# Optimization experiments

Measured on AMD Instinct MI355X. Metric: run time of the kernel, lower is better.

## Reference

```python
import jax, jax.numpy as jnp
import numpy as np

N = 98304        # total nodes (= 16384 graphs * act_dim 6)
E = 1572864      # edges (avg degree 16)
C = 64           # in_channels
H = 32           # hidden_size
ACT = 6          # act_dim


def setup_inputs() -> dict:
    key = jax.random.key(0)
    ks = jax.random.split(key, 11)
    s = lambda fan: 1.0 / np.sqrt(fan)
    return {
        "state": jax.random.normal(ks[0], (N, C), jnp.float32),
        "edge_index": jax.random.randint(ks[1], (2, E), 0, N, dtype=jnp.int64),
        "conv_W": jax.random.normal(ks[2], (C, C), jnp.float32) * s(C),
        "conv_b": jax.random.normal(ks[3], (C,), jnp.float32) * 0.01,
        "W1": jax.random.normal(ks[4], (C, H), jnp.float32) * s(C),
        "b1": jax.random.normal(ks[5], (H,), jnp.float32) * 0.01,
        "W2": jax.random.normal(ks[6], (H, H), jnp.float32) * s(H),
        "b2": jax.random.normal(ks[7], (H,), jnp.float32) * 0.01,
        "W3": jax.random.normal(ks[8], (H, 1), jnp.float32) * s(H),
        "b3": jax.random.normal(ks[9], (1,), jnp.float32) * 0.01,
    }


def gcn_conv(x, edge_index, W, b):
    # PyG GCNConv: add self-loops, symmetric normalization D^-1/2 (A+I) D^-1/2 (X W) + b
    loops = jnp.arange(N, dtype=edge_index.dtype)
    src = jnp.concatenate([edge_index[0], loops])  # [E+N]
    dst = jnp.concatenate([edge_index[1], loops])  # [E+N]
    deg = jax.ops.segment_sum(jnp.ones(E + N, x.dtype), dst, num_segments=N)
    dinv = jax.lax.rsqrt(deg)                      # deg >= 1 due to self-loops
    norm = dinv[src] * dinv[dst]                   # [E+N]
    h = x @ W                                      # [N, C]
    msg = h[src] * norm[:, None]                   # gather + scale
    return jax.ops.segment_sum(msg, dst, num_segments=N) + b


def reference(state, edge_index, conv_W, conv_b, W1, b1, W2, b2, W3, b3):
    out = jax.nn.relu(gcn_conv(state, edge_index, conv_W, conv_b))
    x = out + state                                # residual
    x = x.reshape(-1, ACT, C)                      # [num_graphs, act_dim, C]
    x = jax.nn.relu(x @ W1 + b1)
    x = jax.nn.relu(x @ W2 + b2)
    x = jax.nn.softplus(x @ W3 + b3)
    concentration = x.squeeze(-1) + 1e-20          # [num_graphs, act_dim]
    return concentration
```

## Files before the change

kernel.cpp:

```cpp
#include <hip/hip_runtime.h>
#include <math.h>

#define Nn 98304
#define Ee 1572864
#define Cc 64
#define Hh 32
#define TT 128
#define NT (Nn / TT)
#define HB 128
#define EPB (Ee / HB)
#define CAPT 2560


__device__ __forceinline__ int detect64(const void* ei) {
    const unsigned int* u = (const unsigned int*)ei;
    int is64 = 1;
    #pragma unroll
    for (int i = 0; i < 16; ++i) is64 &= (u[2 * i + 1] == 0u);
    return is64;
}

__device__ __forceinline__ int load_idx(const void* ei, long e, int is64) {
    if (is64) return (int)((const long long*)ei)[e];
    return ((const int*)ei)[e];
}

__device__ __forceinline__ unsigned short f2bf(float x) {
    union { float f; unsigned int u; } v; v.f = x;
    unsigned int r = v.u + 0x7FFFu + ((v.u >> 16) & 1u);
    return (unsigned short)(r >> 16);
}
__device__ __forceinline__ float bf2f(unsigned short h) {
    union { unsigned int u; float f; } v; v.u = ((unsigned int)h) << 16;
    return v.f;
}

__global__ __launch_bounds__(1024) void k_bucket(const void* __restrict__ ei,
                                                 unsigned int* __restrict__ aux,
                                                 unsigned int* __restrict__ ebuf) {
    __shared__ unsigned int hl[NT];
    __shared__ unsigned int off[NT];
    int t = threadIdx.x, b = blockIdx.x;
    if (t < NT) hl[t] = 0;
    __syncthreads();
    int is64 = detect64(ei);
    long e0 = (long)b * EPB;
    #pragma unroll
    for (int i = 0; i < EPB / 1024; ++i) {
        int d = load_idx(ei, (long)Ee + e0 + i * 1024 + t, is64);
        atomicAdd(&hl[d >> 7], 1u);
    }
    __syncthreads();
    if (t < NT) off[t] = hl[t];
    __syncthreads();
    for (int s = 1; s < NT; s <<= 1) {
        unsigned int v = (t < NT && t >= s) ? off[t - s] : 0u;
        __syncthreads();
        if (t < NT) off[t] += v;
        __syncthreads();
    }
    if (t < NT) {
        unsigned int ex = off[t] - hl[t];
        aux[(long)b * NT + t] = ex | (hl[t] << 16);
        off[t] = ex;
    }
    __syncthreads();
    #pragma unroll
    for (int i = 0; i < EPB / 1024; ++i) {
        long e = e0 + i * 1024 + t;
        int s = load_idx(ei, e, is64);
        int d = load_idx(ei, (long)Ee + e, is64);
        unsigned int pos = atomicAdd(&off[d >> 7], 1u);
        ebuf[(long)b * EPB + pos] = (unsigned int)s | ((unsigned int)(d & (TT - 1)) << 17);
    }
}

__global__ __launch_bounds__(256) void k_nodecnt(const unsigned int* __restrict__ aux,
                                                 const unsigned int* __restrict__ ebuf,
                                                 unsigned int* __restrict__ rowOff,
                                                 unsigned int* __restrict__ rowEnd,
                                                 float* __restrict__ dinv,
                                                 unsigned int* __restrict__ srcs) {
    __shared__ unsigned int stage[CAPT];
    __shared__ unsigned int rbI[HB];
    __shared__ unsigned int ro[HB];
    __shared__ unsigned int cnt[TT];
    __shared__ unsigned int sc[TT];
    __shared__ unsigned int cur[TT];
    int t = threadIdx.x, tile = blockIdx.x;
    if (t < HB) {
        unsigned int av = aux[(long)t * NT + tile];
        ro[t] = av & 0xFFFFu;
        rbI[t] = av >> 16;
    }
    __syncthreads();
    for (int s = 1; s < HB; s <<= 1) {
        unsigned int v = (t < HB && t >= s) ? rbI[t - s] : 0u;
        __syncthreads();
        if (t < HB) rbI[t] += v;
        __syncthreads();
    }
    int total = (int)rbI[HB - 1];
    for (int i = t; i < total; i += 256) {
        int pos = 0;
        #pragma unroll
        for (int s = HB / 2; s > 0; s >>= 1)
            if ((int)rbI[pos + s - 1] <= i) pos += s;
        unsigned int prev = pos ? rbI[pos - 1] : 0u;
        stage[i] = ebuf[(long)pos * EPB + ro[pos] + (unsigned int)i - prev];
    }
    if (t < TT) cnt[t] = 0;
    __syncthreads();
    for (int i = t; i < total; i += 256)
        atomicAdd(&cnt[stage[i] >> 17], 1u);
    __syncthreads();
    if (t < TT) sc[t] = cnt[t];
    __syncthreads();
    #pragma unroll
    for (int off = 1; off < TT; off <<= 1) {
        unsigned int v = (t >= off && t < TT) ? sc[t - off] : 0u;
        __syncthreads();
        if (t < TT) sc[t] += v;
        __syncthreads();
    }
    if (t < TT) {
        unsigned int start = (unsigned int)(tile * CAPT) + sc[t] - cnt[t];
        rowOff[(long)tile * TT + t] = start;
        rowEnd[(long)tile * TT + t] = start + cnt[t];
        cur[t] = start;
        dinv[(long)tile * TT + t] = rsqrtf((float)(cnt[t] + 1));
    }
    __syncthreads();
    for (int i = t; i < total; i += 256) {
        unsigned int u = stage[i];
        unsigned int pos = atomicAdd(&cur[u >> 17], 1u);
        srcs[pos] = u & 0x1FFFFu;
    }
}

__global__ __launch_bounds__(256) void k_gemm(const float* __restrict__ state,
                                              const float* __restrict__ W,
                                              const float* __restrict__ dinv,
                                              unsigned short* __restrict__ gb) {
    __shared__ float Wl[64 * 64];
    __shared__ float Al[64 * 68];
    int t = threadIdx.x;
    long n0 = (long)blockIdx.x * 64;

    const float4* W4 = (const float4*)W;
    float4* Wl4 = (float4*)Wl;
    #pragma unroll
    for (int i = 0; i < 4; ++i) Wl4[i * 256 + t] = W4[i * 256 + t];

    const float4* S4 = (const float4*)(state) + n0 * 16;
    #pragma unroll
    for (int i = 0; i < 4; ++i) {
        int f4 = t + i * 256;
        int r = f4 >> 4, k0 = (f4 & 15) * 4;
        *(float4*)(Al + r * 68 + k0) = S4[f4];
    }
    __syncthreads();

    int r0 = (t >> 4) * 4;
    int c0 = (t & 15) * 4;
    float acc[4][4] = {{0.f}};
    #pragma unroll
    for (int kk = 0; kk < 64; kk += 4) {
        float4 a4[4], w4[4];
        #pragma unroll
        for (int i = 0; i < 4; ++i) a4[i] = *(const float4*)(Al + (r0 + i) * 68 + kk);
        #pragma unroll
        for (int j = 0; j < 4; ++j) w4[j] = *(const float4*)(Wl + (kk + j) * 64 + c0);
        const float* aa = (const float*)a4;
        const float* ww = (const float*)w4;
        #pragma unroll
        for (int i = 0; i < 4; ++i)
            #pragma unroll
            for (int j = 0; j < 4; ++j) {
                float av = aa[i * 4 + j];
                #pragma unroll
                for (int c = 0; c < 4; ++c)
                    acc[i][c] = fmaf(av, ww[j * 4 + c], acc[i][c]);
            }
    }
    #pragma unroll
    for (int i = 0; i < 4; ++i) {
        long n = n0 + r0 + i;
        float dv = dinv[n];
        ushort4 o;
        o.x = f2bf(acc[i][0] * dv); o.y = f2bf(acc[i][1] * dv);
        o.z = f2bf(acc[i][2] * dv); o.w = f2bf(acc[i][3] * dv);
        *(ushort4*)(gb + n * 64 + c0) = o;
    }
}

__global__ __launch_bounds__(256) void k_gather(const unsigned int* __restrict__ rowOff,
                                                const unsigned int* __restrict__ rowEnd,
                                                const unsigned int* __restrict__ srcs,
                                                const unsigned short* __restrict__ gb,
                                                const float* __restrict__ dinv,
                                                float* __restrict__ agg) {
    int wave = threadIdx.x >> 6, lane = threadIdx.x & 63;
    int n = blockIdx.x * 4 + wave;
    int start = (int)rowOff[n];
    int end = (int)rowEnd[n];
    float acc = bf2f(gb[(long)n * 64 + lane]);
    for (int base = start; base < end; base += 64) {
        int m = min(64, end - base);
        int sv = (lane < m) ? (int)srcs[base + lane] : 0;
        int j = 0;
        for (; j + 8 <= m; j += 8) {
            int s0 = __shfl(sv, j,     64);
            int s1 = __shfl(sv, j + 1, 64);
            int s2 = __shfl(sv, j + 2, 64);
            int s3 = __shfl(sv, j + 3, 64);
            int s4 = __shfl(sv, j + 4, 64);
            int s5 = __shfl(sv, j + 5, 64);
            int s6 = __shfl(sv, j + 6, 64);
            int s7 = __shfl(sv, j + 7, 64);
            float v0 = bf2f(gb[(long)s0 * 64 + lane]);
            float v1 = bf2f(gb[(long)s1 * 64 + lane]);
            float v2 = bf2f(gb[(long)s2 * 64 + lane]);
            float v3 = bf2f(gb[(long)s3 * 64 + lane]);
            float v4 = bf2f(gb[(long)s4 * 64 + lane]);
            float v5 = bf2f(gb[(long)s5 * 64 + lane]);
            float v6 = bf2f(gb[(long)s6 * 64 + lane]);
            float v7 = bf2f(gb[(long)s7 * 64 + lane]);
            acc += ((v0 + v1) + (v2 + v3)) + ((v4 + v5) + (v6 + v7));
        }
        for (; j + 4 <= m; j += 4) {
            int s0 = __shfl(sv, j,     64);
            int s1 = __shfl(sv, j + 1, 64);
            int s2 = __shfl(sv, j + 2, 64);
            int s3 = __shfl(sv, j + 3, 64);
            float v0 = bf2f(gb[(long)s0 * 64 + lane]);
            float v1 = bf2f(gb[(long)s1 * 64 + lane]);
            float v2 = bf2f(gb[(long)s2 * 64 + lane]);
            float v3 = bf2f(gb[(long)s3 * 64 + lane]);
            acc += (v0 + v1) + (v2 + v3);
        }
        for (; j < m; ++j) {
            int s = __shfl(sv, j, 64);
            acc += bf2f(gb[(long)s * 64 + lane]);
        }
    }
    agg[(long)n * 64 + lane] = acc * dinv[n];
}

__global__ __launch_bounds__(256) void k_final(const float* __restrict__ agg,
                                               const float* __restrict__ state,
                                               const float* __restrict__ conv_b,
                                               const float* __restrict__ W1,
                                               const float* __restrict__ b1,
                                               const float* __restrict__ W2,
                                               const float* __restrict__ b2,
                                               const float* __restrict__ W3,
                                               const float* __restrict__ b3,
                                               float* __restrict__ out) {
    __shared__ float sW1[Cc * Hh];
    __shared__ float sW2[Hh * Hh];
    __shared__ float sW3[Hh], sb1[Hh], sb2[Hh], scb[Cc];
    __shared__ float sb3;
    int t = threadIdx.x;
    for (int i = t; i < Cc * Hh; i += 256) sW1[i] = W1[i];
    for (int i = t; i < Hh * Hh; i += 256) sW2[i] = W2[i];
    if (t < Hh) { sW3[t] = W3[t]; sb1[t] = b1[t]; sb2[t] = b2[t]; }
    if (t < Cc) scb[t] = conv_b[t];
    if (t == 0) sb3 = b3[0];
    __syncthreads();

    int n = blockIdx.x * 256 + t;
    const float4* a4p = (const float4*)(agg + (long)n * 64);
    const float4* s4p = (const float4*)(state + (long)n * 64);
    float x[Cc];
    #pragma unroll
    for (int k4 = 0; k4 < 16; ++k4) {
        float4 a = a4p[k4];
        float4 s = s4p[k4];
        x[k4 * 4 + 0] = fmaxf(a.x + scb[k4 * 4 + 0], 0.f) + s.x;
        x[k4 * 4 + 1] = fmaxf(a.y + scb[k4 * 4 + 1], 0.f) + s.y;
        x[k4 * 4 + 2] = fmaxf(a.z + scb[k4 * 4 + 2], 0.f) + s.z;
        x[k4 * 4 + 3] = fmaxf(a.w + scb[k4 * 4 + 3], 0.f) + s.w;
    }
    float h1[Hh];
    #pragma unroll
    for (int j = 0; j < Hh; ++j) h1[j] = sb1[j];
    #pragma unroll
    for (int k = 0; k < Cc; ++k) {
        float xv = x[k];
        #pragma unroll
        for (int j = 0; j < Hh; ++j) h1[j] = fmaf(xv, sW1[k * Hh + j], h1[j]);
    }
    #pragma unroll
    for (int j = 0; j < Hh; ++j) h1[j] = fmaxf(h1[j], 0.f);

    float h2[Hh];
    #pragma unroll
    for (int j = 0; j < Hh; ++j) h2[j] = sb2[j];
    #pragma unroll
    for (int k = 0; k < Hh; ++k) {
        float xv = h1[k];
        #pragma unroll
        for (int j = 0; j < Hh; ++j) h2[j] = fmaf(xv, sW2[k * Hh + j], h2[j]);
    }
    float y = sb3;
    #pragma unroll
    for (int j = 0; j < Hh; ++j) y = fmaf(fmaxf(h2[j], 0.f), sW3[j], y);

    float sp = fmaxf(y, 0.f) + log1pf(expf(-fabsf(y)));
    out[n] = sp + 1e-20f;
}

extern "C" void kernel_launch(void* const* d_in, const int* in_sizes, int n_in,
                              void* d_out, int out_size, void* d_ws, size_t ws_size,
                              hipStream_t stream) {
    const float* state  = (const float*)d_in[0];
    const void*  ei     = d_in[1];
    const float* conv_W = (const float*)d_in[2];
    const float* conv_b = (const float*)d_in[3];
    const float* W1 = (const float*)d_in[4];
    const float* b1 = (const float*)d_in[5];
    const float* W2 = (const float*)d_in[6];
    const float* b2 = (const float*)d_in[7];
    const float* W3 = (const float*)d_in[8];
    const float* b3 = (const float*)d_in[9];
    float* out = (float*)d_out;

    float*          dinv   = (float*)d_ws;
    unsigned short* gb     = (unsigned short*)(dinv + Nn);
    unsigned int*   rowOff = (unsigned int*)(gb + (size_t)Nn * 64);
    unsigned int*   rowEnd = rowOff + Nn;
    unsigned int*   aux    = rowEnd + Nn;
    unsigned int*   ebuf   = aux + (size_t)HB * NT;
    unsigned int*   srcs   = ebuf + Ee;
    float*          agg    = (float*)(srcs + (size_t)NT * CAPT);

    k_bucket<<<HB, 1024, 0, stream>>>(ei, aux, ebuf);
    k_nodecnt<<<NT, 256, 0, stream>>>(aux, ebuf, rowOff, rowEnd, dinv, srcs);
    k_gemm<<<Nn / 64, 256, 0, stream>>>(state, conv_W, dinv, gb);
    k_gather<<<Nn / 4, 256, 0, stream>>>(rowOff, rowEnd, srcs, gb, dinv, agg);
    k_final<<<Nn / 256, 256, 0, stream>>>(agg, state, conv_b,
                                          W1, b1, W2, b2, W3, b3, out);
}
```

Baseline: 205.3 us.

## Replace per-node CSR gather with per-tile LDS atomic scatter aggregation

Removes the per-node CSR build (the staging pass, the scan and the srcs scatter). Degrees are now counted straight from the bucketed edges. Aggregation runs one 1024-thread block per 128-node tile: it reads the bucketed edges and atomically adds gathered bf16 rows into an LDS accumulator, then writes scaled results. The change also doubles the number of bucket blocks and halves the final kernel's block size. Shared-memory float atomics and a nondeterministic summation order replace the register accumulation, and the block-level edge decoding is redone inside the tile kernel.

Result: slower. 687.8 us (+235.1%).

```diff
diff --git a/kernel.cpp b/kernel.cpp
--- a/kernel.cpp
+++ b/kernel.cpp
@@ -7,9 +7,8 @@
 #define Hh 32
 #define TT 128
 #define NT (Nn / TT)
-#define HB 128
+#define HB 256
 #define EPB (Ee / HB)
-#define CAPT 2560
 
 
 __device__ __forceinline__ int detect64(const void* ei) {
@@ -75,24 +74,19 @@
     }
 }
 
-__global__ __launch_bounds__(256) void k_nodecnt(const unsigned int* __restrict__ aux,
-                                                 const unsigned int* __restrict__ ebuf,
-                                                 unsigned int* __restrict__ rowOff,
-                                                 unsigned int* __restrict__ rowEnd,
-                                                 float* __restrict__ dinv,
-                                                 unsigned int* __restrict__ srcs) {
-    __shared__ unsigned int stage[CAPT];
+__global__ __launch_bounds__(256) void k_deg(const unsigned int* __restrict__ aux,
+                                             const unsigned int* __restrict__ ebuf,
+                                             float* __restrict__ dinv) {
     __shared__ unsigned int rbI[HB];
     __shared__ unsigned int ro[HB];
     __shared__ unsigned int cnt[TT];
-    __shared__ unsigned int sc[TT];
-    __shared__ unsigned int cur[TT];
     int t = threadIdx.x, tile = blockIdx.x;
     if (t < HB) {
         unsigned int av = aux[(long)t * NT + tile];
         ro[t] = av & 0xFFFFu;
         rbI[t] = av >> 16;
     }
+    if (t < TT) cnt[t] = 0;
     __syncthreads();
     for (int s = 1; s < HB; s <<= 1) {
         unsigned int v = (t < HB && t >= s) ? rbI[t - s] : 0u;
@@ -107,35 +101,12 @@
         for (int s = HB / 2; s > 0; s >>= 1)
             if ((int)rbI[pos + s - 1] <= i) pos += s;
         unsigned int prev = pos ? rbI[pos - 1] : 0u;
-        stage[i] = ebuf[(long)pos * EPB + ro[pos] + (unsigned int)i - prev];
-    }
-    if (t < TT) cnt[t] = 0;
-    __syncthreads();
-    for (int i = t; i < total; i += 256)
-        atomicAdd(&cnt[stage[i] >> 17], 1u);
-    __syncthreads();
-    if (t < TT) sc[t] = cnt[t];
-    __syncthreads();
-    #pragma unroll
-    for (int off = 1; off < TT; off <<= 1) {
-        unsigned int v = (t >= off && t < TT) ? sc[t - off] : 0u;
-        __syncthreads();
-        if (t < TT) sc[t] += v;
-        __syncthreads();
-    }
-    if (t < TT) {
-        unsigned int start = (unsigned int)(tile * CAPT) + sc[t] - cnt[t];
-        rowOff[(long)tile * TT + t] = start;
-        rowEnd[(long)tile * TT + t] = start + cnt[t];
-        cur[t] = start;
+        unsigned int u = ebuf[(long)pos * EPB + ro[pos] + (unsigned int)i - prev];
+        atomicAdd(&cnt[u >> 17], 1u);
+    }
+    __syncthreads();
+    if (t < TT)
         dinv[(long)tile * TT + t] = rsqrtf((float)(cnt[t] + 1));
-    }
-    __syncthreads();
-    for (int i = t; i < total; i += 256) {
-        unsigned int u = stage[i];
-        unsigned int pos = atomicAdd(&cur[u >> 17], 1u);
-        srcs[pos] = u & 0x1FFFFu;
-    }
 }
 
 __global__ __launch_bounds__(256) void k_gemm(const float* __restrict__ state,
@@ -194,60 +165,84 @@
     }
 }
 
-__global__ __launch_bounds__(256) void k_gather(const unsigned int* __restrict__ rowOff,
-                                                const unsigned int* __restrict__ rowEnd,
-                                                const unsigned int* __restrict__ srcs,
-                                                const unsigned short* __restrict__ gb,
-                                                const float* __restrict__ dinv,
-                                                float* __restrict__ agg) {
-    int wave = threadIdx.x >> 6, lane = threadIdx.x & 63;
-    int n = blockIdx.x * 4 + wave;
-    int start = (int)rowOff[n];
-    int end = (int)rowEnd[n];
-    float acc = bf2f(gb[(long)n * 64 + lane]);
-    for (int base = start; base < end; base += 64) {
-        int m = min(64, end - base);
-        int sv = (lane < m) ? (int)srcs[base + lane] : 0;
+__global__ __launch_bounds__(1024) void k_tile(const unsigned int* __restrict__ aux,
+                                               const unsigned int* __restrict__ ebuf,
+                                               const unsigned short* __restrict__ gb,
+                                               const float* __restrict__ dinv,
+                                               float* __restrict__ agg) {
+    __shared__ float acc[TT * 64];
+    __shared__ unsigned int rbI[HB];
+    __shared__ unsigned int ro[HB];
+    int t = threadIdx.x, tile = blockIdx.x;
+    int wave = t >> 6, lane = t & 63;
+    long nbase = (long)tile * TT;
+    if (t < HB) {
+        unsigned int av = aux[(long)t * NT + tile];
+        ro[t] = av & 0xFFFFu;
+        rbI[t] = av >> 16;
+    }
+    #pragma unroll
+    for (int i = 0; i < TT * 64 / 1024; ++i)
+        acc[i * 1024 + t] = bf2f(gb[nbase * 64 + i * 1024 + t]);
+    __syncthreads();
+    for (int s = 1; s < HB; s <<= 1) {
+        unsigned int v = (t < HB && t >= s) ? rbI[t - s] : 0u;
+        __syncthreads();
+        if (t < HB) rbI[t] += v;
+        __syncthreads();
+    }
+    int total = (int)rbI[HB - 1];
+    for (int base = wave * 64; base < total; base += 1024) {
+        int m = min(64, total - base);
+        int i = min(base + lane, total - 1);
+        int pos = 0;
+        #pragma unroll
+        for (int s = HB / 2; s > 0; s >>= 1)
+            if ((int)rbI[pos + s - 1] <= i) pos += s;
+        unsigned int prev = pos ? rbI[pos - 1] : 0u;
+        unsigned int ev = ebuf[(long)pos * EPB + ro[pos] + (unsigned int)i - prev];
         int j = 0;
         for (; j + 8 <= m; j += 8) {
-            int s0 = __shfl(sv, j,     64);
-            int s1 = __shfl(sv, j + 1, 64);
-            int s2 = __shfl(sv, j + 2, 64);
-            int s3 = __shfl(sv, j + 3, 64);
-            int s4 = __shfl(sv, j + 4, 64);
-            int s5 = __shfl(sv, j + 5, 64);
-            int s6 = __shfl(sv, j + 6, 64);
-            int s7 = __shfl(sv, j + 7, 64);
-            float v0 = bf2f(gb[(long)s0 * 64 + lane]);
-            float v1 = bf2f(gb[(long)s1 * 64 + lane]);
-            float v2 = bf2f(gb[(long)s2 * 64 + lane]);
-            float v3 = bf2f(gb[(long)s3 * 64 + lane]);
-            float v4 = bf2f(gb[(long)s4 * 64 + lane]);
-            float v5 = bf2f(gb[(long)s5 * 64 + lane]);
-            float v6 = bf2f(gb[(long)s6 * 64 + lane]);
-            float v7 = bf2f(gb[(long)s7 * 64 + lane]);
-            acc += ((v0 + v1) + (v2 + v3)) + ((v4 + v5) + (v6 + v7));
-        }
-        for (; j + 4 <= m; j += 4) {
-            int s0 = __shfl(sv, j,     64);
-            int s1 = __shfl(sv, j + 1, 64);
-            int s2 = __shfl(sv, j + 2, 64);
-            int s3 = __shfl(sv, j + 3, 64);
-            float v0 = bf2f(gb[(long)s0 * 64 + lane]);
-            float v1 = bf2f(gb[(long)s1 * 64 + lane]);
-            float v2 = bf2f(gb[(long)s2 * 64 + lane]);
-            float v3 = bf2f(gb[(long)s3 * 64 + lane]);
-            acc += (v0 + v1) + (v2 + v3);
+            unsigned int u0 = __shfl(ev, j,     64);
+            unsigned int u1 = __shfl(ev, j + 1, 64);
+            unsigned int u2 = __shfl(ev, j + 2, 64);
+            unsigned int u3 = __shfl(ev, j + 3, 64);
+            unsigned int u4 = __shfl(ev, j + 4, 64);
+            unsigned int u5 = __shfl(ev, j + 5, 64);
+            unsigned int u6 = __shfl(ev, j + 6, 64);
+            unsigned int u7 = __shfl(ev, j + 7, 64);
+            float v0 = bf2f(gb[(long)(u0 & 0x1FFFF) * 64 + lane]);
+            float v1 = bf2f(gb[(long)(u1 & 0x1FFFF) * 64 + lane]);
+            float v2 = bf2f(gb[(long)(u2 & 0x1FFFF) * 64 + lane]);
+            float v3 = bf2f(gb[(long)(u3 & 0x1FFFF) * 64 + lane]);
+            float v4 = bf2f(gb[(long)(u4 & 0x1FFFF) * 64 + lane]);
+            float v5 = bf2f(gb[(long)(u5 & 0x1FFFF) * 64 + lane]);
+            float v6 = bf2f(gb[(long)(u6 & 0x1FFFF) * 64 + lane]);
+            float v7 = bf2f(gb[(long)(u7 & 0x1FFFF) * 64 + lane]);
+            unsafeAtomicAdd(&acc[(u0 >> 17) * 64 + lane], v0);
+            unsafeAtomicAdd(&acc[(u1 >> 17) * 64 + lane], v1);
+            unsafeAtomicAdd(&acc[(u2 >> 17) * 64 + lane], v2);
+            unsafeAtomicAdd(&acc[(u3 >> 17) * 64 + lane], v3);
+            unsafeAtomicAdd(&acc[(u4 >> 17) * 64 + lane], v4);
+            unsafeAtomicAdd(&acc[(u5 >> 17) * 64 + lane], v5);
+            unsafeAtomicAdd(&acc[(u6 >> 17) * 64 + lane], v6);
+            unsafeAtomicAdd(&acc[(u7 >> 17) * 64 + lane], v7);
         }
         for (; j < m; ++j) {
-            int s = __shfl(sv, j, 64);
-            acc += bf2f(gb[(long)s * 64 + lane]);
+            unsigned int u = __shfl(ev, j, 64);
+            float v = bf2f(gb[(long)(u & 0x1FFFF) * 64 + lane]);
+            unsafeAtomicAdd(&acc[(u >> 17) * 64 + lane], v);
         }
     }
-    agg[(long)n * 64 + lane] = acc * dinv[n];
-}
-
-__global__ __launch_bounds__(256) void k_final(const float* __restrict__ agg,
+    __syncthreads();
+    #pragma unroll
+    for (int i = 0; i < TT * 64 / 1024; ++i) {
+        int idx = i * 1024 + t;
+        agg[nbase * 64 + idx] = acc[idx] * dinv[nbase + (idx >> 6)];
+    }
+}
+
+__global__ __launch_bounds__(128) void k_final(const float* __restrict__ agg,
                                                const float* __restrict__ state,
                                                const float* __restrict__ conv_b,
                                                const float* __restrict__ W1,
@@ -262,14 +257,14 @@
     __shared__ float sW3[Hh], sb1[Hh], sb2[Hh], scb[Cc];
     __shared__ float sb3;
     int t = threadIdx.x;
-    for (int i = t; i < Cc * Hh; i += 256) sW1[i] = W1[i];
-    for (int i = t; i < Hh * Hh; i += 256) sW2[i] = W2[i];
+    for (int i = t; i < Cc * Hh; i += 128) sW1[i] = W1[i];
+    for (int i = t; i < Hh * Hh; i += 128) sW2[i] = W2[i];
     if (t < Hh) { sW3[t] = W3[t]; sb1[t] = b1[t]; sb2[t] = b2[t]; }
-    if (t < Cc) scb[t] = conv_b[t];
-    if (t == 0) sb3 = b3[0];
-    __syncthreads();
-
-    int n = blockIdx.x * 256 + t;
+    if (t >= 32 && t < 96) scb[t - 32] = conv_b[t - 32];
+    if (t == 127) sb3 = b3[0];
+    __syncthreads();
+
+    int n = blockIdx.x * 128 + t;
     const float4* a4p = (const float4*)(agg + (long)n * 64);
     const float4* s4p = (const float4*)(state + (long)n * 64);
     float x[Cc];
@@ -326,19 +321,16 @@
     const float* b3 = (const float*)d_in[9];
     float* out = (float*)d_out;
 
-    float*          dinv   = (float*)d_ws;
-    unsigned short* gb     = (unsigned short*)(dinv + Nn);
-    unsigned int*   rowOff = (unsigned int*)(gb + (size_t)Nn * 64);
-    unsigned int*   rowEnd = rowOff + Nn;
-    unsigned int*   aux    = rowEnd + Nn;
-    unsigned int*   ebuf   = aux + (size_t)HB * NT;
-    unsigned int*   srcs   = ebuf + Ee;
-    float*          agg    = (float*)(srcs + (size_t)NT * CAPT);
+    float*          dinv = (float*)d_ws;
+    unsigned short* gb   = (unsigned short*)(dinv + Nn);
+    unsigned int*   aux  = (unsigned int*)(gb + (size_t)Nn * 64);
+    unsigned int*   ebuf = aux + (size_t)HB * NT;
+    float*          agg  = (float*)(ebuf + Ee);
 
     k_bucket<<<HB, 1024, 0, stream>>>(ei, aux, ebuf);
-    k_nodecnt<<<NT, 256, 0, stream>>>(aux, ebuf, rowOff, rowEnd, dinv, srcs);
+    k_deg<<<NT, 256, 0, stream>>>(aux, ebuf, dinv);
     k_gemm<<<Nn / 64, 256, 0, stream>>>(state, conv_W, dinv, gb);
-    k_gather<<<Nn / 4, 256, 0, stream>>>(rowOff, rowEnd, srcs, gb, dinv, agg);
-    k_final<<<Nn / 256, 256, 0, stream>>>(agg, state, conv_b,
+    k_tile<<<NT, 1024, 0, stream>>>(aux, ebuf, gb, dinv, agg);
+    k_final<<<Nn / 128, 128, 0, stream>>>(agg, state, conv_b,
                                           W1, b1, W2, b2, W3, b3, out);
 }
```
